# Optimization experiments

Hardware: AMD Instinct MI355X
Metric: run time of the kernel (lower is better)

## Reference

```python
import jax, jax.numpy as jnp
import numpy as np

VOCAB, EMB, LAYERS, OUT, N = 32000, 43, 64, 15, 524288

def setup_inputs() -> dict:
    key = jax.random.key(0)
    ks = jax.random.split(key, 8)
    emb = jax.random.normal(ks[0], (VOCAB, EMB), jnp.float32) * 0.1
    emb = emb.at[0].set(0.0)  # padding_idx=0
    return {
        "tokens": jax.random.randint(ks[1], (N,), 0, VOCAB, jnp.int32),
        "emb": emb,
        "w_ih": jax.random.normal(ks[2], (LAYERS, 4 * EMB, EMB), jnp.float32) * 0.1,
        "w_hh": jax.random.normal(ks[3], (LAYERS, 4 * EMB, EMB), jnp.float32) * 0.1,
        "b_ih": jax.random.normal(ks[4], (LAYERS, 4 * EMB), jnp.float32) * 0.1,
        "b_hh": jax.random.normal(ks[5], (LAYERS, 4 * EMB), jnp.float32) * 0.1,
        "w_out": jax.random.normal(ks[6], (OUT, EMB), jnp.float32) * 0.1,
        "b_out": jax.random.normal(ks[7], (OUT,), jnp.float32) * 0.1,
    }

def reference(tokens, emb, w_ih, w_hh, b_ih, b_hh, w_out, b_out):
    # embedding lookup; dropout is identity in eval mode
    x = emb[tokens]  # (N, EMB)

    # 64-layer LSTM stack, seq_len=1, h0=c0=0 => f-gate * c_prev and W_hh @ h_prev vanish,
    # but we implement the full PyTorch LSTM cell math (gate order i, f, g, o).
    def layer(h, params):
        wi, wh, bi, bh = params
        h_prev = jnp.zeros_like(h)  # initial hidden state per layer
        gates = h @ wi.T + bi + h_prev @ wh.T + bh  # (N, 4*EMB)
        i, f, g, o = jnp.split(gates, 4, axis=-1)
        c = jax.nn.sigmoid(f) * 0.0 + jax.nn.sigmoid(i) * jnp.tanh(g)
        h_new = jax.nn.sigmoid(o) * jnp.tanh(c)
        return h_new, None

    h, _ = jax.lax.scan(layer, x, (w_ih, w_hh, b_ih, b_hh))
    logits = h @ w_out.T + b_out  # (N, OUT)
    return jax.nn.log_softmax(logits, axis=1)
```

## Files before the change

kernel.cpp:

```cpp
#include <hip/hip_runtime.h>

#define LAYERS 64
#define EMBD   43
#define NOUT   15
#define NTOK   524288

#define ROWB     128
#define WROWS    144
#define IMGBYTES (WROWS * ROWB)
#define NCHUNK   18

#define MBLK    256
#define THREADS 256

#define NEG_L2E   -1.44269504f
#define NEG_2L2E  -2.88539008f

typedef short bf16x8 __attribute__((ext_vector_type(8)));
typedef float f32x4  __attribute__((ext_vector_type(4)));

__device__ __forceinline__ unsigned short f2bf(float f) {
  unsigned int u = __builtin_bit_cast(unsigned int, f);
  u = u + 0x7fffu + ((u >> 16) & 1u);
  return (unsigned short)(u >> 16);
}
__device__ __forceinline__ float bf2f(unsigned short s) {
  unsigned int u = ((unsigned int)s) << 16;
  return __builtin_bit_cast(float, u);
}

__global__ void pack_w_kernel(const float* __restrict__ w_ih,
                              const float* __restrict__ b_ih,
                              const float* __restrict__ b_hh,
                              unsigned char* __restrict__ wpack) {
  int idx = blockIdx.x * blockDim.x + threadIdx.x;
  if (idx >= LAYERS * WROWS) return;
  int l = idx / WROWS, n = idx % WROWS;
  int t = n >> 4, c = n & 15;
  int G = t / 3, gidx = t % 3;
  int gsel = (gidx == 0) ? 0 : ((gidx == 1) ? 2 : 3);
  float scale = (gidx == 1) ? NEG_2L2E : NEG_L2E;
  int j = (G == 0) ? 2 * c : ((G == 1) ? 2 * c + 1 : 32 + c);
  int valid = (j < EMBD);
  const float* src = w_ih + ((size_t)l * 172 + (size_t)gsel * EMBD + j) * EMBD;
  float bias = 0.0f;
  if (valid) {
    int R = gsel * EMBD + j;
    bias = (b_ih[l * 172 + R] + b_hh[l * 172 + R]) * scale;
  }
  unsigned char* dst = wpack + (size_t)l * IMGBYTES + n * ROWB;
  #pragma unroll
  for (int g = 0; g < 8; ++g) {
    union { unsigned short s[8]; uint4 v; } pk;
    #pragma unroll
    for (int e = 0; e < 8; ++e) {
      int k = g * 8 + e;
      unsigned short val = 0;
      if (valid && k < EMBD) val = f2bf(src[k] * scale);
      else if (valid && k == EMBD) val = f2bf(bias);
      pk.s[e] = val;
    }
    int slot = g ^ (n & 7);
    *(uint4*)(dst + slot * 16) = pk.v;
  }
}

__global__ void __launch_bounds__(THREADS, 3) lstm_kernel(
    const int* __restrict__ tokens,
    const float* __restrict__ emb,
    const unsigned char* __restrict__ wpack,
    const float* __restrict__ w_out,
    const float* __restrict__ b_out,
    float* __restrict__ out) {
  __shared__ __align__(16) unsigned char Hs[MBLK * ROWB];
  __shared__ __align__(16) unsigned char Ws[IMGBYTES];

  const int tid  = threadIdx.x;
  const int lane = tid & 63;
  const int wave = tid >> 6;
  const int c    = lane & 15;
  const int q    = lane >> 4;
  const int row_base = blockIdx.x * MBLK;

  {
    const unsigned char* src = wpack;
    #pragma unroll
    for (int ch = 0; ch < 5; ++ch) {
      int chunk = wave + ch * 4;
      if (chunk < NCHUNK)
        __builtin_amdgcn_global_load_lds(
            (const __attribute__((address_space(1))) void*)(src + chunk * 1024 + lane * 16),
            (__attribute__((address_space(3))) void*)(Ws + chunk * 1024),
            16, 0, 0);
    }
  }

  {
    int r = tid;
    int tok = tokens[row_base + r];
    const float* e = emb + (size_t)tok * EMBD;
    unsigned short v[64];
    #pragma unroll
    for (int k = 0; k < EMBD; ++k) v[k] = f2bf(e[k]);
    v[EMBD] = 0x3F80;
    #pragma unroll
    for (int k = EMBD + 1; k < 64; ++k) v[k] = 0;
    #pragma unroll
    for (int g = 0; g < 8; ++g) {
      union { unsigned short s[8]; uint4 u; } pk;
      #pragma unroll
      for (int e2 = 0; e2 < 8; ++e2) pk.s[e2] = v[g * 8 + e2];
      *(uint4*)(Hs + r * ROWB + ((g ^ (r & 7)) * 16)) = pk.u;
    }
  }

  int adrA0, adrA1, adrB0, adrB1, adrP[4], adrS[4];
  {
    int ra = wave * 64 + c;
    adrA0 = ra * ROWB + ((q ^ (c & 7)) * 16);
    adrA1 = ra * ROWB + (((4 + q) ^ (c & 7)) * 16);
    adrB0 = c * ROWB + ((q ^ (c & 7)) * 16);
    adrB1 = c * ROWB + (((4 + q) ^ (c & 7)) * 16);
    #pragma unroll
    for (int r4 = 0; r4 < 4; ++r4) {
      int rq = q * 4 + r4;
      int rm = rq & 7;
      int rr = wave * 64 + rq;
      adrP[r4] = rr * ROWB + (((c >> 2) ^ rm) * 16) + (c & 3) * 4;
      adrS[r4] = rr * ROWB + (((4 + (c >> 3)) ^ rm) * 16) + (c & 7) * 2;
    }
  }
  __syncthreads();

  const f32x4 zf = {0.0f, 0.0f, 0.0f, 0.0f};

  #pragma unroll 1
  for (int l = 0; l < LAYERS; ++l) {
    bf16x8 A0[4], A1[4];
    #pragma unroll
    for (int st = 0; st < 4; ++st) {
      A0[st] = *(const bf16x8*)(Hs + adrA0 + st * 2048);
      A1[st] = *(const bf16x8*)(Hs + adrA1 + st * 2048);
    }

    float hh[16];

    #pragma unroll
    for (int G = 0; G < 3; ++G) {
      f32x4 acc[3][4];
      #pragma unroll
      for (int t2 = 0; t2 < 3; ++t2) {
        int off = (G * 3 + t2) * 2048;
        bf16x8 B0 = *(const bf16x8*)(Ws + adrB0 + off);
        #pragma unroll
        for (int st = 0; st < 4; ++st)
          acc[t2][st] = __builtin_amdgcn_mfma_f32_16x16x32_bf16(A0[st], B0, zf, 0, 0, 0);
      }
      #pragma unroll
      for (int t2 = 0; t2 < 3; ++t2) {
        int off = (G * 3 + t2) * 2048;
        bf16x8 B1 = *(const bf16x8*)(Ws + adrB1 + off);
        #pragma unroll
        for (int st = 0; st < 4; ++st)
          acc[t2][st] = __builtin_amdgcn_mfma_f32_16x16x32_bf16(A1[st], B1, acc[t2][st], 0, 0, 0);
      }

      if (G == 2) {
        __syncthreads();
        if (l + 1 < LAYERS) {
          const unsigned char* src = wpack + (size_t)(l + 1) * IMGBYTES;
          #pragma unroll
          for (int ch = 0; ch < 5; ++ch) {
            int chunk = wave + ch * 4;
            if (chunk < NCHUNK)
              __builtin_amdgcn_global_load_lds(
                  (const __attribute__((address_space(1))) void*)(src + chunk * 1024 + lane * 16),
                  (__attribute__((address_space(3))) void*)(Ws + chunk * 1024),
                  16, 0, 0);
          }
        }
      }

      #pragma unroll
      for (int st = 0; st < 4; ++st) {
        #pragma unroll
        for (int r4 = 0; r4 < 4; ++r4) {
          float t1 = __builtin_amdgcn_exp2f(acc[0][st][r4]);
          float t2 = __builtin_amdgcn_exp2f(acc[1][st][r4]);
          float u  = 1.0f + t2;
          float rd = __builtin_amdgcn_rcpf(__builtin_fmaf(t1, u, u));
          float a  = __builtin_fmaf(u, 2.88539008f, -5.77078016f) * rd;
          float t4 = __builtin_amdgcn_exp2f(a);
          float t3 = __builtin_amdgcn_exp2f(acc[2][st][r4]);
          float u2 = 1.0f + t4;
          float rd2 = __builtin_amdgcn_rcpf(__builtin_fmaf(t3, u2, u2));
          float h  = (2.0f - u2) * rd2;
          if (G == 0) {
            hh[st * 4 + r4] = h;
          } else if (G == 1) {
            unsigned int u0 = __builtin_bit_cast(unsigned int, hh[st * 4 + r4]) + 0x8000u;
            unsigned int u1 = __builtin_bit_cast(unsigned int, h) + 0x8000u;
            unsigned int pk = __builtin_amdgcn_perm(u1, u0, 0x07060302u);
            *(unsigned int*)(Hs + adrP[r4] + st * 2048) = pk;
          } else if (c <= 10) {
            unsigned int u1 = (__builtin_bit_cast(unsigned int, h) + 0x8000u) >> 16;
            *(unsigned short*)(Hs + adrS[r4] + st * 2048) = (unsigned short)u1;
          }
        }
      }
    }
    __syncthreads();
  }

  {
    int r = tid;
    float h[EMBD];
    #pragma unroll
    for (int g = 0; g < 6; ++g) {
      union { uint4 u; unsigned short s[8]; } pk;
      pk.u = *(const uint4*)(Hs + r * ROWB + ((g ^ (r & 7)) * 16));
      #pragma unroll
      for (int e2 = 0; e2 < 8; ++e2) {
        int k = g * 8 + e2;
        if (k < EMBD) h[k] = bf2f(pk.s[e2]);
      }
    }
    float logit[NOUT];
    #pragma unroll
    for (int o = 0; o < NOUT; ++o) {
      float sum = b_out[o];
      #pragma unroll
      for (int k = 0; k < EMBD; ++k) sum += w_out[o * EMBD + k] * h[k];
      logit[o] = sum;
    }
    float m = logit[0];
    #pragma unroll
    for (int o = 1; o < NOUT; ++o) m = fmaxf(m, logit[o]);
    float ss = 0.0f;
    #pragma unroll
    for (int o = 0; o < NOUT; ++o) ss += __expf(logit[o] - m);
    float lse = m + __logf(ss);
    float* dst = out + (size_t)(row_base + r) * NOUT;
    #pragma unroll
    for (int o = 0; o < NOUT; ++o) dst[o] = logit[o] - lse;
  }
}

extern "C" void kernel_launch(void* const* d_in, const int* in_sizes, int n_in,
                              void* d_out, int out_size, void* d_ws, size_t ws_size,
                              hipStream_t stream) {
  const int* tokens     = (const int*)d_in[0];
  const float* emb      = (const float*)d_in[1];
  const float* w_ih     = (const float*)d_in[2];
  const float* b_ih     = (const float*)d_in[4];
  const float* b_hh     = (const float*)d_in[5];
  const float* w_out    = (const float*)d_in[6];
  const float* b_out    = (const float*)d_in[7];
  float* out            = (float*)d_out;

  const size_t need = (size_t)LAYERS * IMGBYTES;
  unsigned char* wpack = (ws_size >= need) ? (unsigned char*)d_ws
                                           : (unsigned char*)d_in[3];

  pack_w_kernel<<<(LAYERS * WROWS + 255) / 256, 256, 0, stream>>>(w_ih, b_ih, b_hh, wpack);
  lstm_kernel<<<NTOK / MBLK, THREADS, 0, stream>>>(tokens, emb, wpack, w_out, b_out, out);
}
```

Baseline: 1.153 ms.

## Shrink LDS row stride to 112 bytes, drop swizzle, double block size

Shared-memory rows go from 128 to 112 bytes: only 48 bf16 columns are stored and the XOR swizzle is dropped. The upper half of the second MFMA K-slice is read from a shared zero buffer, so the padding columns are never stored. The block grows to 512 rows and 512 threads with launch bounds of 4, and the weight image becomes 16 KB loaded in two rounds. The goal is less LDS per row and more rows per block for occupancy, at the risk of bank conflicts from the unswizzled 112-byte stride and branchy pointer selection for the zero reads.

```diff
diff --git a/kernel.cpp b/kernel.cpp
--- a/kernel.cpp
+++ b/kernel.cpp
@@ -5,13 +5,13 @@
 #define NOUT   15
 #define NTOK   524288
 
-#define ROWB     128
+#define ROWB     112
 #define WROWS    144
-#define IMGBYTES (WROWS * ROWB)
-#define NCHUNK   18
-
-#define MBLK    256
-#define THREADS 256
+#define IMGBYTES 16384
+#define NCHUNK   16
+
+#define MBLK    512
+#define THREADS 512
 
 #define NEG_L2E   -1.44269504f
 #define NEG_2L2E  -2.88539008f
@@ -50,7 +50,7 @@
   }
   unsigned char* dst = wpack + (size_t)l * IMGBYTES + n * ROWB;
   #pragma unroll
-  for (int g = 0; g < 8; ++g) {
+  for (int g = 0; g < 6; ++g) {
     union { unsigned short s[8]; uint4 v; } pk;
     #pragma unroll
     for (int e = 0; e < 8; ++e) {
@@ -60,12 +60,11 @@
       else if (valid && k == EMBD) val = f2bf(bias);
       pk.s[e] = val;
     }
-    int slot = g ^ (n & 7);
-    *(uint4*)(dst + slot * 16) = pk.v;
-  }
-}
-
-__global__ void __launch_bounds__(THREADS, 3) lstm_kernel(
+    *(uint4*)(dst + g * 16) = pk.v;
+  }
+}
+
+__global__ void __launch_bounds__(THREADS, 4) lstm_kernel(
     const int* __restrict__ tokens,
     const float* __restrict__ emb,
     const unsigned char* __restrict__ wpack,
@@ -74,6 +73,7 @@
     float* __restrict__ out) {
   __shared__ __align__(16) unsigned char Hs[MBLK * ROWB];
   __shared__ __align__(16) unsigned char Ws[IMGBYTES];
+  __shared__ __align__(16) float Zb[4];
 
   const int tid  = threadIdx.x;
   const int lane = tid & 63;
@@ -82,16 +82,17 @@
   const int q    = lane >> 4;
   const int row_base = blockIdx.x * MBLK;
 
+  if (tid == 0) { Zb[0] = 0.0f; Zb[1] = 0.0f; Zb[2] = 0.0f; Zb[3] = 0.0f; }
+
   {
     const unsigned char* src = wpack;
     #pragma unroll
-    for (int ch = 0; ch < 5; ++ch) {
-      int chunk = wave + ch * 4;
-      if (chunk < NCHUNK)
-        __builtin_amdgcn_global_load_lds(
-            (const __attribute__((address_space(1))) void*)(src + chunk * 1024 + lane * 16),
-            (__attribute__((address_space(3))) void*)(Ws + chunk * 1024),
-            16, 0, 0);
+    for (int rnd = 0; rnd < 2; ++rnd) {
+      int chunk = wave + rnd * 8;
+      __builtin_amdgcn_global_load_lds(
+          (const __attribute__((address_space(1))) void*)(src + chunk * 1024 + lane * 16),
+          (__attribute__((address_space(3))) void*)(Ws + chunk * 1024),
+          16, 0, 0);
     }
   }
 
@@ -99,36 +100,40 @@
     int r = tid;
     int tok = tokens[row_base + r];
     const float* e = emb + (size_t)tok * EMBD;
-    unsigned short v[64];
+    unsigned short v[48];
     #pragma unroll
     for (int k = 0; k < EMBD; ++k) v[k] = f2bf(e[k]);
     v[EMBD] = 0x3F80;
     #pragma unroll
-    for (int k = EMBD + 1; k < 64; ++k) v[k] = 0;
-    #pragma unroll
-    for (int g = 0; g < 8; ++g) {
+    for (int k = EMBD + 1; k < 48; ++k) v[k] = 0;
+    #pragma unroll
+    for (int g = 0; g < 6; ++g) {
       union { unsigned short s[8]; uint4 u; } pk;
       #pragma unroll
       for (int e2 = 0; e2 < 8; ++e2) pk.s[e2] = v[g * 8 + e2];
-      *(uint4*)(Hs + r * ROWB + ((g ^ (r & 7)) * 16)) = pk.u;
-    }
-  }
-
-  int adrA0, adrA1, adrB0, adrB1, adrP[4], adrS[4];
-  {
-    int ra = wave * 64 + c;
-    adrA0 = ra * ROWB + ((q ^ (c & 7)) * 16);
-    adrA1 = ra * ROWB + (((4 + q) ^ (c & 7)) * 16);
-    adrB0 = c * ROWB + ((q ^ (c & 7)) * 16);
-    adrB1 = c * ROWB + (((4 + q) ^ (c & 7)) * 16);
-    #pragma unroll
-    for (int r4 = 0; r4 < 4; ++r4) {
-      int rq = q * 4 + r4;
-      int rm = rq & 7;
-      int rr = wave * 64 + rq;
-      adrP[r4] = rr * ROWB + (((c >> 2) ^ rm) * 16) + (c & 3) * 4;
-      adrS[r4] = rr * ROWB + (((4 + (c >> 3)) ^ rm) * 16) + (c & 7) * 2;
-    }
+      *(uint4*)(Hs + r * ROWB + g * 16) = pk.u;
+    }
+  }
+
+  const int adrA  = (wave * 64 + c) * ROWB;
+  const int adrA0 = adrA + 16 * q;
+  const int adrB0 = c * ROWB + 16 * q;
+  const unsigned char* pA1[4];
+  const unsigned char* pB1[9];
+  #pragma unroll
+  for (int st = 0; st < 4; ++st)
+    pA1[st] = (q < 2) ? (Hs + adrA + st * 1792 + 64 + 16 * q)
+                      : (const unsigned char*)Zb;
+  #pragma unroll
+  for (int t = 0; t < 9; ++t)
+    pB1[t] = (q < 2) ? (Ws + c * ROWB + t * 1792 + 64 + 16 * q)
+                     : (const unsigned char*)Zb;
+  int adrP[4], adrS[4];
+  #pragma unroll
+  for (int r4 = 0; r4 < 4; ++r4) {
+    int rr = wave * 64 + q * 4 + r4;
+    adrP[r4] = rr * ROWB + 4 * c;
+    adrS[r4] = rr * ROWB + 64 + 2 * c;
   }
   __syncthreads();
 
@@ -139,8 +144,8 @@
     bf16x8 A0[4], A1[4];
     #pragma unroll
     for (int st = 0; st < 4; ++st) {
-      A0[st] = *(const bf16x8*)(Hs + adrA0 + st * 2048);
-      A1[st] = *(const bf16x8*)(Hs + adrA1 + st * 2048);
+      A0[st] = *(const bf16x8*)(Hs + adrA0 + st * 1792);
+      A1[st] = *(const bf16x8*)(pA1[st]);
     }
 
     float hh[16];
@@ -150,16 +155,14 @@
       f32x4 acc[3][4];
       #pragma unroll
       for (int t2 = 0; t2 < 3; ++t2) {
-        int off = (G * 3 + t2) * 2048;
-        bf16x8 B0 = *(const bf16x8*)(Ws + adrB0 + off);
+        bf16x8 B0 = *(const bf16x8*)(Ws + adrB0 + (G * 3 + t2) * 1792);
         #pragma unroll
         for (int st = 0; st < 4; ++st)
           acc[t2][st] = __builtin_amdgcn_mfma_f32_16x16x32_bf16(A0[st], B0, zf, 0, 0, 0);
       }
       #pragma unroll
       for (int t2 = 0; t2 < 3; ++t2) {
-        int off = (G * 3 + t2) * 2048;
-        bf16x8 B1 = *(const bf16x8*)(Ws + adrB1 + off);
+        bf16x8 B1 = *(const bf16x8*)(pB1[G * 3 + t2]);
         #pragma unroll
         for (int st = 0; st < 4; ++st)
           acc[t2][st] = __builtin_amdgcn_mfma_f32_16x16x32_bf16(A1[st], B1, acc[t2][st], 0, 0, 0);
@@ -170,13 +173,12 @@
         if (l + 1 < LAYERS) {
           const unsigned char* src = wpack + (size_t)(l + 1) * IMGBYTES;
           #pragma unroll
-          for (int ch = 0; ch < 5; ++ch) {
-            int chunk = wave + ch * 4;
-            if (chunk < NCHUNK)
-              __builtin_amdgcn_global_load_lds(
-                  (const __attribute__((address_space(1))) void*)(src + chunk * 1024 + lane * 16),
-                  (__attribute__((address_space(3))) void*)(Ws + chunk * 1024),
-                  16, 0, 0);
+          for (int rnd = 0; rnd < 2; ++rnd) {
+            int chunk = wave + rnd * 8;
+            __builtin_amdgcn_global_load_lds(
+                (const __attribute__((address_space(1))) void*)(src + chunk * 1024 + lane * 16),
+                (__attribute__((address_space(3))) void*)(Ws + chunk * 1024),
+                16, 0, 0);
           }
         }
       }
@@ -201,10 +203,10 @@
             unsigned int u0 = __builtin_bit_cast(unsigned int, hh[st * 4 + r4]) + 0x8000u;
             unsigned int u1 = __builtin_bit_cast(unsigned int, h) + 0x8000u;
             unsigned int pk = __builtin_amdgcn_perm(u1, u0, 0x07060302u);
-            *(unsigned int*)(Hs + adrP[r4] + st * 2048) = pk;
+            *(unsigned int*)(Hs + adrP[r4] + st * 1792) = pk;
           } else if (c <= 10) {
             unsigned int u1 = (__builtin_bit_cast(unsigned int, h) + 0x8000u) >> 16;
-            *(unsigned short*)(Hs + adrS[r4] + st * 2048) = (unsigned short)u1;
+            *(unsigned short*)(Hs + adrS[r4] + st * 1792) = (unsigned short)u1;
           }
         }
       }
@@ -218,7 +220,7 @@
     #pragma unroll
     for (int g = 0; g < 6; ++g) {
       union { uint4 u; unsigned short s[8]; } pk;
-      pk.u = *(const uint4*)(Hs + r * ROWB + ((g ^ (r & 7)) * 16));
+      pk.u = *(const uint4*)(Hs + r * ROWB + g * 16);
       #pragma unroll
       for (int e2 = 0; e2 < 8; ++e2) {
         int k = g * 8 + e2;
```

New measurement: 1.183 ms. 2.6% more time.
